# Optimization experiments

Hardware: AMD Instinct MI355X
Metric: run time of the kernel (lower is better)

## Reference

```python
import jax, jax.numpy as jnp
import numpy as np
import math

B, T, C = 2, 2048, 2048
NH = 16
HS = C // NH

def setup_inputs() -> dict:
    key = jax.random.key(0)
    k1, k2, k3 = jax.random.split(key, 3)
    x = jax.random.normal(k1, (B, T, C), dtype=jnp.float32)
    w_attn = jax.random.normal(k2, (3 * C, C), dtype=jnp.float32) * 0.02
    w_proj = jax.random.normal(k3, (C, C), dtype=jnp.float32) * 0.02
    return {"x": x, "w_attn": w_attn, "w_proj": w_proj}

def reference(x, w_attn, w_proj):
    Bx, Tx, Cx = x.shape
    # qkv projection: Linear(C, 3C), no bias
    qkv = jnp.einsum('btc,oc->bto', x, w_attn)  # [B,T,3C]
    q, k, v = jnp.split(qkv, 3, axis=-1)
    # reshape to heads: [B,T,H,hs]
    q = q.reshape(Bx, Tx, NH, HS)
    k = k.reshape(Bx, Tx, NH, HS)
    v = v.reshape(Bx, Tx, NH, HS)
    # scores [B,H,Tq,Tk]
    att = jnp.einsum('bqhd,bkhd->bhqk', q, k) * (1.0 / math.sqrt(HS))
    causal = jnp.tril(jnp.ones((Tx, Tx), dtype=bool))
    att = jnp.where(causal[None, None], att, -jnp.inf)
    att = jax.nn.softmax(att, axis=-1)
    # attn_dropout with p=0.0 is identity
    y = jnp.einsum('bhqk,bkhd->bqhd', att, v)
    y = y.reshape(Bx, Tx, Cx)
    return jnp.einsum('btc,oc->bto', y, w_proj)
```

## Files before the change

### kernel.cpp

```cpp
#include <hip/hip_runtime.h>

typedef __attribute__((ext_vector_type(8))) short short8;
typedef __attribute__((ext_vector_type(4))) float f32x4;
typedef unsigned short u16;

#define T_SEQ 2048
#define C_DIM 2048

static __device__ __forceinline__ u16 f2bf(float f){
  unsigned u = __float_as_uint(f);
  u = (u + 0x7fffu + ((u >> 16) & 1u)) >> 16;
  return (u16)u;
}

__global__ void cvt3_kernel(const float* __restrict__ x,
                            const float* __restrict__ wa,
                            const float* __restrict__ wp,
                            u16* __restrict__ xb, u16* __restrict__ wab,
                            u16* __restrict__ wpb){
  int idx = blockIdx.x * blockDim.x + threadIdx.x;
  int stride = gridDim.x * blockDim.x;
  for (int i = idx; i < 6291456; i += stride){
    const float* src; u16* dst; int j;
    if (i < 2097152){ src = x;  dst = xb;  j = i; }
    else if (i < 5242880){ src = wa; dst = wab; j = i - 2097152; }
    else { src = wp; dst = wpb; j = i - 5242880; }
    float4 v = ((const float4*)src)[j];
    ushort4 o;
    o.x = f2bf(v.x); o.y = f2bf(v.y); o.z = f2bf(v.z); o.w = f2bf(v.w);
    ((ushort4*)dst)[j] = o;
  }
}

__device__ __forceinline__ void gl_lds16(const void* g, void* l){
  __builtin_amdgcn_global_load_lds(
      (const __attribute__((address_space(1))) unsigned int*)g,
      (__attribute__((address_space(3))) unsigned int*)l,
      16, 0, 0);
}

template<int MODE, typename OUT>
__global__ __launch_bounds__(256) void gemm_bt(const u16* __restrict__ A,
                                               const u16* __restrict__ B,
                                               OUT* __restrict__ C,
                                               u16* __restrict__ VT,
                                               int M, int N, int K){
  __shared__ __align__(16) u16 lA[2][128*32];
  __shared__ __align__(16) u16 lB[2][128*32];
  const int tid  = threadIdx.x;
  const int lane = tid & 63;
  const int r16  = lane & 15;
  const int g4   = lane >> 4;
  const int wave = tid >> 6;
  const int wr = (wave >> 1) * 64, wc = (wave & 1) * 64;

  const int nwg = gridDim.x * gridDim.y;
  const int idl = blockIdx.y * gridDim.x + blockIdx.x;
  const int wg  = (idl & 7) * (nwg >> 3) + (idl >> 3);
  const int bx  = wg / gridDim.y, by = wg % gridDim.y;
  const int m0 = by * 128, n0 = bx * 128;

  const int srow = tid >> 2;
  const int scol = (tid & 3) << 3;

  f32x4 acc[4][4] = {};

  const int nk = K >> 5;
  int buf = 0;

  gl_lds16(&A[(size_t)(m0 + srow)*K + scol],      &lA[0][srow*32 + scol]);
  gl_lds16(&A[(size_t)(m0 + 64 + srow)*K + scol], &lA[0][(64+srow)*32 + scol]);
  gl_lds16(&B[(size_t)(n0 + srow)*K + scol],      &lB[0][srow*32 + scol]);
  gl_lds16(&B[(size_t)(n0 + 64 + srow)*K + scol], &lB[0][(64+srow)*32 + scol]);

  for (int kt = 0; kt < nk; ++kt){
    __syncthreads();
    if (kt + 1 < nk){
      const int k0 = (kt + 1) << 5;
      gl_lds16(&A[(size_t)(m0 + srow)*K + k0 + scol],      &lA[buf^1][srow*32 + scol]);
      gl_lds16(&A[(size_t)(m0 + 64 + srow)*K + k0 + scol], &lA[buf^1][(64+srow)*32 + scol]);
      gl_lds16(&B[(size_t)(n0 + srow)*K + k0 + scol],      &lB[buf^1][srow*32 + scol]);
      gl_lds16(&B[(size_t)(n0 + 64 + srow)*K + k0 + scol], &lB[buf^1][(64+srow)*32 + scol]);
    }
    short8 af[4], bfv[4];
    #pragma unroll
    for (int i=0;i<4;i++)
      af[i] = *(const short8*)&lA[buf][(wr + i*16 + r16)*32 + g4*8];
    #pragma unroll
    for (int j=0;j<4;j++)
      bfv[j] = *(const short8*)&lB[buf][(wc + j*16 + r16)*32 + g4*8];
    #pragma unroll
    for (int i=0;i<4;i++)
      #pragma unroll
      for (int j=0;j<4;j++)
        acc[i][j] = __builtin_amdgcn_mfma_f32_16x16x32_bf16(af[i], bfv[j], acc[i][j], 0,0,0);
    buf ^= 1;
  }

  if (MODE == 1 && n0 >= 4096){
    #pragma unroll
    for (int i=0;i<4;i++){
      const int m = m0 + wr + i*16 + g4*4;
      const int bb = m >> 11, t = m & 2047;
      #pragma unroll
      for (int j=0;j<4;j++){
        const int cv = n0 + wc + j*16 + r16 - 4096;
        const int h = cv >> 7, dl = cv & 127;
        ushort4 pack;
        pack.x = f2bf(acc[i][j][0]); pack.y = f2bf(acc[i][j][1]);
        pack.z = f2bf(acc[i][j][2]); pack.w = f2bf(acc[i][j][3]);
        *(ushort4*)&VT[(size_t)((bb<<4) + h)*262144 + (size_t)dl*2048 + t] = pack;
      }
    }
  } else {
    const int ldc = (MODE == 1) ? 4096 : N;
    #pragma unroll
    for (int i=0;i<4;i++){
      const int row = m0 + wr + i*16 + g4*4;
      #pragma unroll
      for (int j=0;j<4;j++){
        const int col = n0 + wc + j*16 + r16;
        #pragma unroll
        for (int r=0;r<4;r++){
          float v = acc[i][j][r];
          if constexpr (sizeof(OUT)==2) C[(size_t)(row+r)*ldc + col] = (OUT)f2bf(v);
          else                          C[(size_t)(row+r)*ldc + col] = (OUT)v;
        }
      }
    }
  }
}

__global__ __launch_bounds__(256) void attn_kernel(const u16* __restrict__ qk,
                                                   const u16* __restrict__ vt,
                                                   u16* __restrict__ y){
  __shared__ __align__(16) u16 Kl[2][64*128];
  __shared__ __align__(16) u16 Vl[2][128*64];
  __shared__ __align__(16) u16 Pl[4][32*64];

  const int tid = threadIdx.x, lane = tid & 63, wave = tid >> 6;
  const int r16 = lane & 15, g4 = lane >> 4;

  const int id = blockIdx.x;
  const int xk = id & 7,  kk = id >> 3;
  const int bh = 4*xk + (kk & 3);
  const int v5 = kk >> 2;
  const int qt = (v5 < 8) ? v5 : (23 - v5);

  const int b = bh >> 4, h = bh & 15;
  const int qcol = h*128, kcol = 2048 + h*128;
  const u16* vhead = vt + (size_t)bh * 262144;
  const float scale = 0.08838834764831845f;

  short8 qf[2][4];
  #pragma unroll
  for (int i=0;i<2;i++){
    const u16* qp = qk + (size_t)(b*T_SEQ + qt*128 + wave*32 + i*16 + r16)*4096 + qcol;
    #pragma unroll
    for (int c=0;c<4;c++) qf[i][c] = *(const short8*)&qp[g4*8 + c*32];
  }

  float mrow[2][4], lrow[2][4];
  #pragma unroll
  for (int i=0;i<2;i++)
    #pragma unroll
    for (int r=0;r<4;r++){ mrow[i][r] = -1e30f; lrow[i][r] = 0.f; }
  f32x4 o[2][8] = {};

  const int nt = 2*qt + 2;

  auto stage = [&](int sbuf, int t){
    const size_t kbase = (size_t)(b*T_SEQ + t*64)*4096 + kcol;
    #pragma unroll
    for (int c=0;c<4;c++){
      const int row0 = wave*16 + c*4;
      const int row  = row0 + g4;
      gl_lds16(&qk[kbase + (size_t)row*4096 + ((r16*8) ^ ((row&7)<<3))],
               &Kl[sbuf][row0*128]);
    }
    const int t0 = t*64;
    #pragma unroll
    for (int c=0;c<4;c++){
      const int idx = wave*4 + c;
      const int d   = idx*8 + (lane>>3);
      const int j8  = (lane&7)*8;
      gl_lds16(&vhead[(size_t)d*2048 + t0 + (j8 ^ ((d&7)<<3))],
               &Vl[sbuf][idx*512]);
    }
  };

  stage(0, 0);
  int cur = 0;

  for (int t = 0; t < nt; ++t){
    __syncthreads();
    if (t + 1 < nt) stage(cur^1, t+1);

    float smat[2][4][4];
    #pragma unroll
    for (int cc=0;cc<4;cc++){
      const int krow = cc*16 + r16;
      const int sw = (krow & 7) << 3;
      short8 kf[4];
      #pragma unroll
      for (int dc=0;dc<4;dc++)
        kf[dc] = *(const short8*)&Kl[cur][krow*128 + ((g4*8 + dc*32) ^ sw)];
      #pragma unroll
      for (int i=0;i<2;i++){
        f32x4 sv = {0.f,0.f,0.f,0.f};
        #pragma unroll
        for (int dc=0;dc<4;dc++)
          sv = __builtin_amdgcn_mfma_f32_16x16x32_bf16(qf[i][dc], kf[dc], sv, 0,0,0);
        #pragma unroll
        for (int rr=0;rr<4;rr++) smat[i][cc][rr] = sv[rr] * scale;
      }
    }
    if (t >= 2*qt){
      #pragma unroll
      for (int cc=0;cc<4;cc++){
        const int kvl = (t - 2*qt)*64 + cc*16 + r16;
        #pragma unroll
        for (int i=0;i<2;i++)
          #pragma unroll
          for (int rr=0;rr<4;rr++){
            const int qi = wave*32 + i*16 + g4*4 + rr;
            if (kvl > qi) smat[i][cc][rr] = -1e30f;
          }
      }
    }

    float pm[2][4];
    #pragma unroll
    for (int i=0;i<2;i++)
      #pragma unroll
      for (int rr=0;rr<4;rr++){
        float p0 = fmaxf(fmaxf(smat[i][0][rr], smat[i][1][rr]),
                         fmaxf(smat[i][2][rr], smat[i][3][rr]));
        #pragma unroll
        for (int off=1; off<16; off<<=1) p0 = fmaxf(p0, __shfl_xor(p0, off, 64));
        pm[i][rr] = p0;
      }
    bool need = false;
    #pragma unroll
    for (int i=0;i<2;i++)
      #pragma unroll
      for (int rr=0;rr<4;rr++) need = need || (pm[i][rr] > mrow[i][rr] + 8.f);
    if (__any(need)){
      #pragma unroll
      for (int i=0;i<2;i++)
        #pragma unroll
        for (int rr=0;rr<4;rr++){
          const float mnew = fmaxf(mrow[i][rr], pm[i][rr]);
          const float corr = __expf(mrow[i][rr] - mnew);
          mrow[i][rr] = mnew;
          lrow[i][rr] *= corr;
          #pragma unroll
          for (int n=0;n<8;n++) o[i][n][rr] *= corr;
        }
    }
    #pragma unroll
    for (int i=0;i<2;i++)
      #pragma unroll
      for (int rr=0;rr<4;rr++){
        float s0 = 0.f;
        #pragma unroll
        for (int cc=0;cc<4;cc++){
          const float p = __expf(smat[i][cc][rr] - mrow[i][rr]);
          smat[i][cc][rr] = p;
          s0 += p;
        }
        #pragma unroll
        for (int off=1; off<16; off<<=1) s0 += __shfl_xor(s0, off, 64);
        lrow[i][rr] += s0;
      }

    #pragma unroll
    for (int i=0;i<2;i++)
      #pragma unroll
      for (int cc=0;cc<4;cc++)
        #pragma unroll
        for (int rr=0;rr<4;rr++){
          const int qr = i*16 + g4*4 + rr;
          Pl[wave][qr*64 + ((cc*16 + r16) ^ ((qr&7)<<3))] = f2bf(smat[i][cc][rr]);
        }
    asm volatile("s_waitcnt lgkmcnt(0)" ::: "memory");

    short8 pf[2][2];
    #pragma unroll
    for (int i=0;i<2;i++){
      const int qr = i*16 + r16;
      const int sw = (qr & 7) << 3;
      pf[i][0] = *(const short8*)&Pl[wave][qr*64 + ((g4*8)      ^ sw)];
      pf[i][1] = *(const short8*)&Pl[wave][qr*64 + ((g4*8 + 32) ^ sw)];
    }
    #pragma unroll
    for (int n=0;n<8;n++){
      const int vr = n*16 + r16;
      const int sw = (vr & 7) << 3;
      short8 vf0 = *(const short8*)&Vl[cur][vr*64 + ((g4*8)      ^ sw)];
      short8 vf1 = *(const short8*)&Vl[cur][vr*64 + ((g4*8 + 32) ^ sw)];
      #pragma unroll
      for (int i=0;i<2;i++){
        o[i][n] = __builtin_amdgcn_mfma_f32_16x16x32_bf16(pf[i][0], vf0, o[i][n], 0,0,0);
        o[i][n] = __builtin_amdgcn_mfma_f32_16x16x32_bf16(pf[i][1], vf1, o[i][n], 0,0,0);
      }
    }
    cur ^= 1;
  }

  #pragma unroll
  for (int i=0;i<2;i++){
    const size_t yr0 = (size_t)(b*T_SEQ + qt*128 + wave*32 + i*16 + g4*4) * C_DIM + h*128;
    #pragma unroll
    for (int n=0;n<8;n++)
      #pragma unroll
      for (int rr=0;rr<4;rr++){
        const float v = o[i][n][rr] / lrow[i][rr];
        y[yr0 + (size_t)rr*C_DIM + n*16 + r16] = f2bf(v);
      }
  }
}

extern "C" void kernel_launch(void* const* d_in, const int* in_sizes, int n_in,
                              void* d_out, int out_size, void* d_ws, size_t ws_size,
                              hipStream_t stream){
  const float* x  = (const float*)d_in[0];
  const float* wa = (const float*)d_in[1];
  const float* wp = (const float*)d_in[2];
  float* out = (float*)d_out;

  u16* ws  = (u16*)d_ws;
  u16* xb  = ws;
  u16* wab = xb  + 8388608;
  u16* wpb = wab + 12582912;
  u16* qk  = wpb + 4194304;
  u16* vt  = qk  + 16777216;
  u16* yb  = xb;

  hipLaunchKernelGGL(cvt3_kernel, dim3(2048), dim3(256), 0, stream,
                     x, wa, wp, xb, wab, wpb);

  hipLaunchKernelGGL((gemm_bt<1,u16>),   dim3(48,32), dim3(256), 0, stream,
                     xb, wab, qk, vt, 4096, 6144, 2048);
  hipLaunchKernelGGL(attn_kernel,        dim3(512),  dim3(256), 0, stream,
                     qk, vt, yb);
  hipLaunchKernelGGL((gemm_bt<0,float>), dim3(16,32), dim3(256), 0, stream,
                     yb, wpb, out, (u16*)nullptr, 4096, 2048, 2048);
}
```

Measured before the change: 306.1 us.

## Replace GEMM with 128x256 tile, 8-wave, XOR-swizzled LDS and split-phase pipeline

Rewrites the projection GEMM to use 128x256 output tiles with 512 threads (8 waves), a K-step of 64, and XOR-swizzled LDS layout to avoid bank conflicts. The loop is split into two half-phases, each issuing the next tile's global-to-LDS loads before MFMA work. Explicit vmcnt waits, barriers, and setprio control the overlap. This aims to raise arithmetic intensity and hide load latency. In exchange it uses more LDS and more registers per block, and halves the grid size, which may reduce occupancy.

Measured after the change: 292.9 us. 4.3% less time.

```diff
diff --git a/kernel.cpp b/kernel.cpp
--- a/kernel.cpp
+++ b/kernel.cpp
@@ -40,86 +40,142 @@
 }
 
 template<int MODE, typename OUT>
-__global__ __launch_bounds__(256) void gemm_bt(const u16* __restrict__ A,
-                                               const u16* __restrict__ B,
-                                               OUT* __restrict__ C,
-                                               u16* __restrict__ VT,
-                                               int M, int N, int K){
-  __shared__ __align__(16) u16 lA[2][128*32];
-  __shared__ __align__(16) u16 lB[2][128*32];
+__global__ __launch_bounds__(512, 2) void gemm256(const u16* __restrict__ A,
+                                                  const u16* __restrict__ B,
+                                                  OUT* __restrict__ C,
+                                                  u16* __restrict__ VT,
+                                                  int M, int N, int K){
+  __shared__ __align__(16) u16 lA[2][128*64];
+  __shared__ __align__(16) u16 lB[2][256*64];
   const int tid  = threadIdx.x;
   const int lane = tid & 63;
   const int r16  = lane & 15;
   const int g4   = lane >> 4;
   const int wave = tid >> 6;
-  const int wr = (wave >> 1) * 64, wc = (wave & 1) * 64;
+  const int wm = wave >> 2, wn = wave & 3;
 
   const int nwg = gridDim.x * gridDim.y;
   const int idl = blockIdx.y * gridDim.x + blockIdx.x;
   const int wg  = (idl & 7) * (nwg >> 3) + (idl >> 3);
   const int bx  = wg / gridDim.y, by = wg % gridDim.y;
-  const int m0 = by * 128, n0 = bx * 128;
-
-  const int srow = tid >> 2;
-  const int scol = (tid & 3) << 3;
+  const int m0 = by * 128, n0 = bx * 256;
 
   f32x4 acc[4][4] = {};
-
-  const int nk = K >> 5;
-  int buf = 0;
-
-  gl_lds16(&A[(size_t)(m0 + srow)*K + scol],      &lA[0][srow*32 + scol]);
-  gl_lds16(&A[(size_t)(m0 + 64 + srow)*K + scol], &lA[0][(64+srow)*32 + scol]);
-  gl_lds16(&B[(size_t)(n0 + srow)*K + scol],      &lB[0][srow*32 + scol]);
-  gl_lds16(&B[(size_t)(n0 + 64 + srow)*K + scol], &lB[0][(64+srow)*32 + scol]);
-
-  for (int kt = 0; kt < nk; ++kt){
-    __syncthreads();
-    if (kt + 1 < nk){
-      const int k0 = (kt + 1) << 5;
-      gl_lds16(&A[(size_t)(m0 + srow)*K + k0 + scol],      &lA[buf^1][srow*32 + scol]);
-      gl_lds16(&A[(size_t)(m0 + 64 + srow)*K + k0 + scol], &lA[buf^1][(64+srow)*32 + scol]);
-      gl_lds16(&B[(size_t)(n0 + srow)*K + k0 + scol],      &lB[buf^1][srow*32 + scol]);
-      gl_lds16(&B[(size_t)(n0 + 64 + srow)*K + k0 + scol], &lB[buf^1][(64+srow)*32 + scol]);
-    }
-    short8 af[4], bfv[4];
+  const int nt = K >> 6;
+
+  auto stA = [&](int b, int t){
+    #pragma unroll
+    for (int c=0;c<2;c++){
+      const int row0 = wave*16 + c*8;
+      const int row  = row0 + (lane>>3);
+      const int cole = (((lane&7) ^ (row&7)) << 3);
+      gl_lds16(&A[(size_t)(m0+row)*K + t*64 + cole], &lA[b][row0*64]);
+    }
+  };
+  auto stB2 = [&](int b, int t, int half){
+    #pragma unroll
+    for (int c=0;c<2;c++){
+      const int row0 = (wave>>1)*64 + half*32 + (wave&1)*16 + c*8;
+      const int row  = row0 + (lane>>3);
+      const int cole = (((lane&7) ^ (row&7)) << 3);
+      gl_lds16(&B[(size_t)(n0+row)*K + t*64 + cole], &lB[b][row0*64]);
+    }
+  };
+  auto rdA = [&](short8 (&af)[4][2], int b){
+    #pragma unroll
+    for (int i=0;i<4;i++){
+      const int R = wm*64 + i*16 + r16;
+      #pragma unroll
+      for (int ks=0;ks<2;ks++)
+        af[i][ks] = *(const short8*)&lA[b][R*64 + ((g4*8 + ks*32) ^ ((R&7)<<3))];
+    }
+  };
+  auto rdB = [&](short8 (&bf)[2][2], int b, int half){
+    #pragma unroll
+    for (int j=0;j<2;j++){
+      const int R = wn*64 + half*32 + j*16 + r16;
+      #pragma unroll
+      for (int ks=0;ks<2;ks++)
+        bf[j][ks] = *(const short8*)&lB[b][R*64 + ((g4*8 + ks*32) ^ ((R&7)<<3))];
+    }
+  };
+
+  stA(0,0); stB2(0,0,0); stB2(0,0,1);
+  asm volatile("s_waitcnt vmcnt(2)" ::: "memory");
+  __builtin_amdgcn_s_barrier();
+  asm volatile("" ::: "memory");
+
+  for (int t = 0; t < nt; ++t){
+    const int cb = t & 1, nb = cb ^ 1;
+    const bool more = (t + 1 < nt);
+    short8 af[4][2], bf[2][2];
+
+    rdA(af, cb); rdB(bf, cb, 0);
+    if (more){
+      stA(nb, t+1); stB2(nb, t+1, 0);
+      asm volatile("s_waitcnt vmcnt(4)" ::: "memory");
+    } else {
+      asm volatile("s_waitcnt vmcnt(0)" ::: "memory");
+    }
+    __builtin_amdgcn_s_barrier();
+    asm volatile("s_waitcnt lgkmcnt(0)" ::: "memory");
+    __builtin_amdgcn_sched_barrier(0);
+    __builtin_amdgcn_s_setprio(1);
     #pragma unroll
     for (int i=0;i<4;i++)
-      af[i] = *(const short8*)&lA[buf][(wr + i*16 + r16)*32 + g4*8];
-    #pragma unroll
-    for (int j=0;j<4;j++)
-      bfv[j] = *(const short8*)&lB[buf][(wc + j*16 + r16)*32 + g4*8];
+      #pragma unroll
+      for (int j=0;j<2;j++)
+        #pragma unroll
+        for (int ks=0;ks<2;ks++)
+          acc[i][j] = __builtin_amdgcn_mfma_f32_16x16x32_bf16(af[i][ks], bf[j][ks], acc[i][j], 0,0,0);
+    __builtin_amdgcn_s_setprio(0);
+    __builtin_amdgcn_s_barrier();
+    asm volatile("" ::: "memory");
+
+    rdB(bf, cb, 1);
+    if (more){
+      stB2(nb, t+1, 1);
+      asm volatile("s_waitcnt vmcnt(2)" ::: "memory");
+    }
+    __builtin_amdgcn_s_barrier();
+    asm volatile("s_waitcnt lgkmcnt(0)" ::: "memory");
+    __builtin_amdgcn_sched_barrier(0);
+    __builtin_amdgcn_s_setprio(1);
     #pragma unroll
     for (int i=0;i<4;i++)
       #pragma unroll
-      for (int j=0;j<4;j++)
-        acc[i][j] = __builtin_amdgcn_mfma_f32_16x16x32_bf16(af[i], bfv[j], acc[i][j], 0,0,0);
-    buf ^= 1;
+      for (int j=0;j<2;j++)
+        #pragma unroll
+        for (int ks=0;ks<2;ks++)
+          acc[i][2+j] = __builtin_amdgcn_mfma_f32_16x16x32_bf16(af[i][ks], bf[j][ks], acc[i][2+j], 0,0,0);
+    __builtin_amdgcn_s_setprio(0);
+    __builtin_amdgcn_s_barrier();
+    asm volatile("" ::: "memory");
   }
 
   if (MODE == 1 && n0 >= 4096){
     #pragma unroll
     for (int i=0;i<4;i++){
-      const int m = m0 + wr + i*16 + g4*4;
-      const int bb = m >> 11, t = m & 2047;
+      const int m = m0 + wm*64 + i*16 + g4*4;
+      const int bb = m >> 11, tt = m & 2047;
       #pragma unroll
       for (int j=0;j<4;j++){
-        const int cv = n0 + wc + j*16 + r16 - 4096;
+        const int cv = n0 + wn*64 + j*16 + r16 - 4096;
         const int h = cv >> 7, dl = cv & 127;
         ushort4 pack;
         pack.x = f2bf(acc[i][j][0]); pack.y = f2bf(acc[i][j][1]);
         pack.z = f2bf(acc[i][j][2]); pack.w = f2bf(acc[i][j][3]);
-        *(ushort4*)&VT[(size_t)((bb<<4) + h)*262144 + (size_t)dl*2048 + t] = pack;
+        *(ushort4*)&VT[(size_t)((bb<<4) + h)*262144 + (size_t)dl*2048 + tt] = pack;
       }
     }
   } else {
     const int ldc = (MODE == 1) ? 4096 : N;
     #pragma unroll
     for (int i=0;i<4;i++){
-      const int row = m0 + wr + i*16 + g4*4;
+      const int row = m0 + wm*64 + i*16 + g4*4;
       #pragma unroll
       for (int j=0;j<4;j++){
-        const int col = n0 + wc + j*16 + r16;
+        const int col = n0 + wn*64 + j*16 + r16;
         #pragma unroll
         for (int r=0;r<4;r++){
           float v = acc[i][j][r];
@@ -340,10 +396,10 @@
   hipLaunchKernelGGL(cvt3_kernel, dim3(2048), dim3(256), 0, stream,
                      x, wa, wp, xb, wab, wpb);
 
-  hipLaunchKernelGGL((gemm_bt<1,u16>),   dim3(48,32), dim3(256), 0, stream,
+  hipLaunchKernelGGL((gemm256<1,u16>),   dim3(24,32), dim3(512), 0, stream,
                      xb, wab, qk, vt, 4096, 6144, 2048);
   hipLaunchKernelGGL(attn_kernel,        dim3(512),  dim3(256), 0, stream,
                      qk, vt, yb);
-  hipLaunchKernelGGL((gemm_bt<0,float>), dim3(16,32), dim3(256), 0, stream,
+  hipLaunchKernelGGL((gemm256<0,float>), dim3(8,32),  dim3(512), 0, stream,
                      yb, wpb, out, (u16*)nullptr, 4096, 2048, 2048);
 }
```
